# Performance work log

Hardware: AMD Instinct MI355X
Metric: run time of the kernel (lower is better)

Reference implementation:

```python
import jax, jax.numpy as jnp
import numpy as np

NUM_HEADS = 16
WINDOW = 512
EPS = 1e-5


def layer_norm(x, g, b):
    m = jnp.mean(x, axis=-1, keepdims=True)
    v = jnp.var(x, axis=-1, keepdims=True)
    return (x - m) * jax.lax.rsqrt(v + EPS) * g + b


def rope(x, pos):
    # x: [B,H,S,D], rotate-half RoPE with base 10000
    D = x.shape[-1]
    inv_freq = 1.0 / (10000.0 ** (jnp.arange(0, D, 2, dtype=jnp.float32) / D))
    ang = pos[:, None].astype(jnp.float32) * inv_freq  # [S, D/2]
    cos = jnp.concatenate([jnp.cos(ang), jnp.cos(ang)], axis=-1)
    sin = jnp.concatenate([jnp.sin(ang), jnp.sin(ang)], axis=-1)
    x1, x2 = jnp.split(x, 2, axis=-1)
    rot = jnp.concatenate([-x2, x1], axis=-1)
    return x * cos + rot * sin


def setup_inputs() -> dict:
    key = jax.random.key(0)
    ks = jax.random.split(key, 8)
    B, S, Dm = 2, 2048, 1024
    Dff = 4 * Dm
    sc = 0.02
    return {
        'hidden_states': jax.random.normal(ks[0], (B, S, Dm), jnp.float32),
        'ln1_g': jnp.ones((Dm,), jnp.float32),
        'ln1_b': jnp.zeros((Dm,), jnp.float32),
        'wq': jax.random.normal(ks[1], (Dm, Dm), jnp.float32) * sc,
        'bq': jnp.zeros((Dm,), jnp.float32),
        'wk': jax.random.normal(ks[2], (Dm, Dm), jnp.float32) * sc,
        'bk': jnp.zeros((Dm,), jnp.float32),
        'wv': jax.random.normal(ks[3], (Dm, Dm), jnp.float32) * sc,
        'bv': jnp.zeros((Dm,), jnp.float32),
        'wo': jax.random.normal(ks[4], (Dm, Dm), jnp.float32) * sc,
        'bo': jnp.zeros((Dm,), jnp.float32),
        'ln2_g': jnp.ones((Dm,), jnp.float32),
        'ln2_b': jnp.zeros((Dm,), jnp.float32),
        'w1': jax.random.normal(ks[5], (Dm, Dff), jnp.float32) * sc,
        'b1': jnp.zeros((Dff,), jnp.float32),
        'w2': jax.random.normal(ks[6], (Dff, Dm), jnp.float32) * sc,
        'b2': jnp.zeros((Dm,), jnp.float32),
        'global_token_indices': jax.random.randint(ks[7], (8,), 0, S, jnp.int32),
    }


def reference(hidden_states, ln1_g, ln1_b, wq, bq, wk, bk, wv, bv, wo, bo,
              ln2_g, ln2_b, w1, b1, w2, b2, global_token_indices):
    B, S, Dm = hidden_states.shape
    H = NUM_HEADS
    Dh = Dm // H

    # --- attention block ---
    x = layer_norm(hidden_states, ln1_g, ln1_b)
    heads = lambda t: t.reshape(B, S, H, Dh).transpose(0, 2, 1, 3)  # [B,H,S,Dh]
    q = heads(x @ wq + bq)
    k = heads(x @ wk + bk)
    v = heads(x @ wv + bv)

    pos = jnp.arange(S)
    q = rope(q, pos)
    k = rope(k, pos)

    scores = jnp.einsum('bhqd,bhkd->bhqk', q, k) / jnp.sqrt(jnp.float32(Dh))
    i = pos[:, None]
    j = pos[None, :]
    causal = j <= i
    band = causal & ((i - j) < WINDOW)
    is_global = jnp.zeros((S,), bool).at[global_token_indices].set(True)
    allowed = band | (causal & (is_global[None, :] | is_global[:, None]))
    scores = jnp.where(allowed[None, None], scores, jnp.float32(-1e9))
    attn = jax.nn.softmax(scores, axis=-1)
    ctx = jnp.einsum('bhqk,bhkd->bhqd', attn, v)
    ctx = ctx.transpose(0, 2, 1, 3).reshape(B, S, Dm)
    attn_out = ctx @ wo + bo
    h = hidden_states + attn_out

    # --- MLP block ---
    y = layer_norm(h, ln2_g, ln2_b)
    mlp = jax.nn.gelu(y @ w1 + b1, approximate=False) @ w2 + b2
    return h + mlp
```

## Files before the change

kernel.cpp:

```cpp
#include <hip/hip_runtime.h>

typedef unsigned short u16;
typedef __bf16 bf16x8 __attribute__((ext_vector_type(8)));
typedef short s16x8 __attribute__((ext_vector_type(8)));
typedef float f32x4 __attribute__((ext_vector_type(4)));

#define NB 2
#define SS 2048
#define DM 1024
#define NH 16
#define DH 64
#define DFF 4096

__device__ __forceinline__ u16 f2bf(float f) {
    unsigned u = __float_as_uint(f);
    u += 0x7fff + ((u >> 16) & 1);
    return (u16)(u >> 16);
}
__device__ __forceinline__ float bf2f(u16 h) {
    return __uint_as_float(((unsigned)h) << 16);
}
__device__ __forceinline__ void gld_lds16(const void* g, void* l) {
    __builtin_amdgcn_global_load_lds(
        (const __attribute__((address_space(1))) unsigned int*)(size_t)g,
        (__attribute__((address_space(3))) unsigned int*)(unsigned)(size_t)l,
        16, 0, 0);
}
__device__ __forceinline__ float gelu_f(float x) {
    return 0.5f * x * (1.f + erff(x * 0.70710678118654752f));
}

__global__ void wtrans_kernel(const float* __restrict__ w, u16* __restrict__ wt,
                              int K, int N) {
    __shared__ unsigned tl[64][65];
    int n0 = blockIdx.x * 64, k0 = blockIdx.y * 64, t = threadIdx.x;
    for (int it = 0; it < 16; ++it) {
        int e = it * 256 + t; int r = e >> 6, c = e & 63;
        tl[r][c] = f2bf(w[(size_t)(k0 + r) * N + n0 + c]);
    }
    __syncthreads();
    for (int it = 0; it < 16; ++it) {
        int e = it * 256 + t; int r = e >> 6, c = e & 63;
        wt[(size_t)(n0 + r) * K + k0 + c] = (u16)tl[c][r];
    }
}

__global__ void wtrans4_kernel(const float* __restrict__ a, const float* __restrict__ b,
                               const float* __restrict__ c, const float* __restrict__ d,
                               u16* __restrict__ oa, u16* __restrict__ ob,
                               u16* __restrict__ oc, u16* __restrict__ od) {
    __shared__ unsigned tl[64][65];
    const float* w; u16* wt;
    switch (blockIdx.z) {
        case 0: w = a; wt = oa; break;
        case 1: w = b; wt = ob; break;
        case 2: w = c; wt = oc; break;
        default: w = d; wt = od; break;
    }
    int n0 = blockIdx.x * 64, k0 = blockIdx.y * 64, t = threadIdx.x;
    for (int it = 0; it < 16; ++it) {
        int e = it * 256 + t; int r = e >> 6, cc = e & 63;
        tl[r][cc] = f2bf(w[(size_t)(k0 + r) * DM + n0 + cc]);
    }
    __syncthreads();
    for (int it = 0; it < 16; ++it) {
        int e = it * 256 + t; int r = e >> 6, cc = e & 63;
        wt[(size_t)(n0 + r) * DM + k0 + cc] = (u16)tl[cc][r];
    }
}

__global__ void build_aux(const int* __restrict__ gti, unsigned long long* __restrict__ kmask,
                          const float* __restrict__ bq, const float* __restrict__ bk,
                          const float* __restrict__ bv, float* __restrict__ bias3) {
    int t = threadIdx.x;
    if (t < 32) {
        unsigned long long m = 0ull;
        #pragma unroll
        for (int i = 0; i < 8; ++i) {
            int g = gti[i];
            if ((g >> 6) == t) m |= 1ull << (g & 63);
        }
        kmask[t] = m;
    }
    for (int i = t; i < 1024; i += 256) {
        bias3[i] = bq[i]; bias3[1024 + i] = bk[i]; bias3[2048 + i] = bv[i];
    }
}

template <bool INIT>
__global__ __launch_bounds__(256) void ln_kernel(const float* __restrict__ x,
                                                 const float* __restrict__ g,
                                                 const float* __restrict__ b,
                                                 u16* __restrict__ out,
                                                 const float* __restrict__ ib,
                                                 float* __restrict__ iout) {
    int row = blockIdx.x, t = threadIdx.x;
    const float4 v = ((const float4*)(x + (size_t)row * DM))[t];
    float s  = v.x + v.y + v.z + v.w;
    float sq = v.x * v.x + v.y * v.y + v.z * v.z + v.w * v.w;
    #pragma unroll
    for (int m = 1; m < 64; m <<= 1) { s += __shfl_xor(s, m); sq += __shfl_xor(sq, m); }
    __shared__ float ss[4], ssq[4];
    int wv = t >> 6, lane = t & 63;
    if (lane == 0) { ss[wv] = s; ssq[wv] = sq; }
    __syncthreads();
    s  = ss[0] + ss[1] + ss[2] + ss[3];
    sq = ssq[0] + ssq[1] + ssq[2] + ssq[3];
    float mean = s * (1.f / DM);
    float var  = sq * (1.f / DM) - mean * mean;
    float rs   = rsqrtf(var + 1e-5f);
    float4 gg = ((const float4*)g)[t];
    float4 bb = ((const float4*)b)[t];
    ushort4 o;
    o.x = f2bf((v.x - mean) * rs * gg.x + bb.x);
    o.y = f2bf((v.y - mean) * rs * gg.y + bb.y);
    o.z = f2bf((v.z - mean) * rs * gg.z + bb.z);
    o.w = f2bf((v.w - mean) * rs * gg.w + bb.w);
    ((ushort4*)(out + (size_t)row * DM))[t] = o;
    if (INIT) {
        float4 b2 = ((const float4*)ib)[t];
        float4 iv; iv.x = v.x + b2.x; iv.y = v.y + b2.y; iv.z = v.z + b2.z; iv.w = v.w + b2.w;
        ((float4*)(iout + (size_t)row * DM))[t] = iv;
    }
}

__global__ __launch_bounds__(256) void rope_kernel(const u16* __restrict__ qkv,
                                                   u16* __restrict__ qh,
                                                   u16* __restrict__ kh) {
    int idx = blockIdx.x * 256 + threadIdx.x;
    int d = idx & 31;
    int s = (idx >> 5) & (SS - 1);
    int h = (idx >> 16) & (NH - 1);
    int b = idx >> 20;
    size_t src = ((size_t)(b * SS + s)) * 3072 + h * DH + d;
    size_t dst = ((size_t)((b * NH + h) * SS + s)) * DH + d;
    float inv = powf(10000.f, -(float)d * (1.f / 32.f));
    float ang = (float)s * inv;
    float sn, cs;
    sincosf(ang, &sn, &cs);
    const float QSC = 0.125f;
    float x1 = bf2f(qkv[src]), x2 = bf2f(qkv[src + 32]);
    qh[dst]      = f2bf((x1 * cs - x2 * sn) * QSC);
    qh[dst + 32] = f2bf((x2 * cs + x1 * sn) * QSC);
    x1 = bf2f(qkv[src + 1024]); x2 = bf2f(qkv[src + 1024 + 32]);
    kh[dst]      = f2bf(x1 * cs - x2 * sn);
    kh[dst + 32] = f2bf(x2 * cs + x1 * sn);
}

__global__ __launch_bounds__(256) void vtrans_kernel(const u16* __restrict__ qkv,
                                                     u16* __restrict__ vt) {
    __shared__ unsigned tile[64][65];
    int st = blockIdx.x, bh = blockIdx.y;
    int b = bh >> 4, h = bh & 15, t = threadIdx.x;
    const u16* src = qkv + ((size_t)b * SS + st * 64) * 3072 + 2048 + h * DH;
    for (int it = 0; it < 16; ++it) {
        int e = it * 256 + t; int r = e >> 6, c = e & 63;
        tile[r][c] = src[(size_t)r * 3072 + c];
    }
    __syncthreads();
    u16* dst = vt + ((size_t)bh * DH) * SS + st * 64;
    for (int it = 0; it < 16; ++it) {
        int e = it * 256 + t; int d = e >> 6, s = e & 63;
        dst[(size_t)d * SS + s] = (u16)tile[s][d];
    }
}

__device__ __forceinline__ void xcd_remap(int& bn, int& bm, int& bz) {
    int s = blockIdx.x + gridDim.x * (blockIdx.y + gridDim.y * blockIdx.z);
    int q = gridDim.y >> 3;
    int xcd = s & 7, lin = s >> 3;
    bm = xcd * q + (lin % q);
    int rest = lin / q;
    bn = rest % gridDim.x;
    bz = rest / gridDim.x;
}

template <int MODE, int REMAP>
__global__ __launch_bounds__(256) void gemm_bt(const u16* __restrict__ A,
                                               const u16* __restrict__ Bt,
                                               const float* __restrict__ bias,
                                               const float* __restrict__ res,
                                               void* __restrict__ Cout,
                                               int M, int N, int K, int ldk) {
    int bnb = blockIdx.x, bmb = blockIdx.y, bzb = blockIdx.z;
    if (REMAP) xcd_remap(bnb, bmb, bzb);
    const int bm = bmb * 128, bn = bnb * 128;
    const int koff = bzb * K;
    const int t = threadIdx.x, wv = t >> 6, lane = t & 63;
    const int lr = lane & 15, lq = lane >> 4;
    const int wm = (wv >> 1) * 64, wn = (wv & 1) * 64;
    __shared__ __align__(16) u16 As[2][128 * 64];
    __shared__ __align__(16) u16 Bs[2][128 * 64];
    f32x4 acc[4][4] = {};

    auto stage = [&](int kb, int buf) {
        #pragma unroll
        for (int p = 0; p < 4; ++p) {
            int c = p * 256 + t;
            int r = c >> 3;
            int gc = ((c & 7) ^ (r & 7)) * 8;
            gld_lds16(A + (size_t)(bm + r) * ldk + kb + gc,
                      As[buf] + (size_t)(p * 256 + wv * 64) * 8);
            gld_lds16(Bt + (size_t)(bn + r) * ldk + kb + gc,
                      Bs[buf] + (size_t)(p * 256 + wv * 64) * 8);
        }
    };

    stage(koff, 0);
    int pb = 0;
    for (int k0 = 0; k0 < K; k0 += 64) {
        __syncthreads();
        if (k0 + 64 < K) stage(koff + k0 + 64, pb ^ 1);
        const u16* Ac = As[pb];
        const u16* Bc = Bs[pb];
        #pragma unroll
        for (int ks = 0; ks < 2; ++ks) {
            bf16x8 af[4], bfr[4];
            #pragma unroll
            for (int mi = 0; mi < 4; ++mi) {
                int row = wm + mi * 16 + lr;
                af[mi] = *(const bf16x8*)&Ac[row * 64 + (((ks * 4 + lq) ^ (row & 7)) * 8)];
            }
            #pragma unroll
            for (int ni = 0; ni < 4; ++ni) {
                int row = wn + ni * 16 + lr;
                bfr[ni] = *(const bf16x8*)&Bc[row * 64 + (((ks * 4 + lq) ^ (row & 7)) * 8)];
            }
            #pragma unroll
            for (int mi = 0; mi < 4; ++mi)
                #pragma unroll
                for (int ni = 0; ni < 4; ++ni)
                    acc[mi][ni] = __builtin_amdgcn_mfma_f32_16x16x32_bf16(af[mi], bfr[ni], acc[mi][ni], 0, 0, 0);
        }
        pb ^= 1;
    }
    #pragma unroll
    for (int mi = 0; mi < 4; ++mi) {
        int row0 = bm + wm + mi * 16 + lq * 4;
        #pragma unroll
        for (int ni = 0; ni < 4; ++ni) {
            int col = bn + wn + ni * 16 + lr;
            float bv = (MODE == 3) ? 0.f : bias[col];
            #pragma unroll
            for (int r = 0; r < 4; ++r) {
                float v = acc[mi][ni][r] + bv;
                size_t off = (size_t)(row0 + r) * N + col;
                if (MODE == 1) v += res[off];
                if (MODE == 2) v = gelu_f(v);
                if (MODE == 0 || MODE == 2) ((u16*)Cout)[off] = f2bf(v);
                else if (MODE == 1)         ((float*)Cout)[off] = v;
                else                        atomicAdd((float*)Cout + off, v);
            }
        }
    }
}

template <int MODE, int REMAP>
__global__ __launch_bounds__(512, 2) void gemm256(const u16* __restrict__ A,
                                                  const u16* __restrict__ Bt,
                                                  const float* __restrict__ bias,
                                                  void* __restrict__ Cout,
                                                  int M, int N, int K, int ldk) {
    int bnb = blockIdx.x, bmb = blockIdx.y, bzb = blockIdx.z;
    if (REMAP) xcd_remap(bnb, bmb, bzb);
    const int bm = bmb * 256, bn = bnb * 256;
    const int t = threadIdx.x, wv = t >> 6, lane = t & 63;
    const int lr = lane & 15, lq = lane >> 4;
    const int wm = (wv >> 2) * 128, wn = (wv & 3) * 64;
    const int awb = (wv >> 2) * 64;
    const int bwb = (wv & 3) * 32;
    __shared__ __align__(16) u16 As[2 * 2 * 128 * 64];
    __shared__ __align__(16) u16 Bs[2 * 2 * 128 * 64];
    f32x4 acc[8][4] = {};
    bf16x8 aA[4][2], bA[2][2], bB[2][2];

    const int aix0 = (awb + lr) * 64 + ((lq ^ (lr & 7)) * 8);
    const int aix1 = aix0 ^ 32;
    const int bix0 = (bwb + lr) * 64 + ((lq ^ (lr & 7)) * 8);
    const int bix1 = bix0 ^ 32;

    const u16 *pAsrc[2][2], *pBsrc[2][2];
    #pragma unroll
    for (int g = 0; g < 2; ++g)
        #pragma unroll
        for (int p = 0; p < 2; ++p) {
            int c = p * 512 + t;
            int glr = c >> 3, sl = c & 7;
            int sc = (sl ^ (glr & 7)) * 8;
            int grA = (glr & 63) + g * 64 + ((glr >> 6) << 7);
            int grB = (glr & 31) + g * 32 + ((glr >> 5) << 6);
            pAsrc[g][p] = A  + (size_t)(bm + grA) * ldk + sc;
            pBsrc[g][p] = Bt + (size_t)(bn + grB) * ldk + sc;
        }
    auto stA = [&](int g, int db, int ku) {
        #pragma unroll
        for (int p = 0; p < 2; ++p)
            gld_lds16(pAsrc[g][p] + ku, As + (size_t)(db * 2 + g) * 8192
                                           + (size_t)(p * 512 + wv * 64) * 8);
    };
    auto stB = [&](int g, int db, int ku) {
        #pragma unroll
        for (int p = 0; p < 2; ++p)
            gld_lds16(pBsrc[g][p] + ku, Bs + (size_t)(db * 2 + g) * 8192
                                           + (size_t)(p * 512 + wv * 64) * 8);
    };
    auto mmac = [&](int qm, int qn, bf16x8 (&bb)[2][2]) {
        __builtin_amdgcn_s_setprio(1);
        #pragma unroll
        for (int mi2 = 0; mi2 < 4; ++mi2)
            #pragma unroll
            for (int ni2 = 0; ni2 < 2; ++ni2)
                #pragma unroll
                for (int ks = 0; ks < 2; ++ks)
                    acc[qm * 4 + mi2][qn * 2 + ni2] =
                        __builtin_amdgcn_mfma_f32_16x16x32_bf16(
                            aA[mi2][ks], bb[ni2][ks], acc[qm * 4 + mi2][qn * 2 + ni2], 0, 0, 0);
        __builtin_amdgcn_s_setprio(0);
    };
    #define BAR       __builtin_amdgcn_s_barrier()
    #define VMW(n)    asm volatile("s_waitcnt vmcnt(" #n ")" ::: "memory")
    #define LOADA(DB, G) do {                                                  \
        constexpr int O_ = ((DB) * 2 + (G)) * 8192;                            \
        aA[0][0] = *(const bf16x8*)&As[aix0 + O_];                             \
        aA[0][1] = *(const bf16x8*)&As[aix1 + O_];                             \
        aA[1][0] = *(const bf16x8*)&As[aix0 + O_ + 1024];                      \
        aA[1][1] = *(const bf16x8*)&As[aix1 + O_ + 1024];                      \
        aA[2][0] = *(const bf16x8*)&As[aix0 + O_ + 2048];                      \
        aA[2][1] = *(const bf16x8*)&As[aix1 + O_ + 2048];                      \
        aA[3][0] = *(const bf16x8*)&As[aix0 + O_ + 3072];                      \
        aA[3][1] = *(const bf16x8*)&As[aix1 + O_ + 3072];                      \
    } while (0)
    #define LOADB(DB, G, DST) do {                                             \
        constexpr int O_ = ((DB) * 2 + (G)) * 8192;                            \
        DST[0][0] = *(const bf16x8*)&Bs[bix0 + O_];                            \
        DST[0][1] = *(const bf16x8*)&Bs[bix1 + O_];                            \
        DST[1][0] = *(const bf16x8*)&Bs[bix0 + O_ + 1024];                     \
        DST[1][1] = *(const bf16x8*)&Bs[bix1 + O_ + 1024];                     \
    } while (0)
    #define G256_TILE(DB, KT) do {                                             \
        const int ku1 = ((KT) + 1) << 6, ku2 = ((KT) + 2) << 6;                \
        LOADA(DB, 0); LOADB(DB, 0, bA);               \
        stA(1, (DB) ^ 1, ku1);                                                 \
        BAR;                                                                   \
        mmac(0, 0, bA);                                                        \
        VMW(6); BAR;                                                           \
        LOADB(DB, 1, bB);                             \
        stB(1, (DB) ^ 1, ku1);                                                 \
        BAR;                                                                   \
        mmac(0, 1, bB);                                                        \
        BAR;                                                                   \
        LOADA(DB, 1);                                 \
        stA(0, DB, ku2);                                                       \
        BAR;                                                                   \
        mmac(1, 1, bB);                                                        \
        BAR;                                                                   \
        stB(0, DB, ku2);                              \
        BAR;                                                                   \
        mmac(1, 0, bA);                                                        \
        VMW(8); BAR;                                                           \
    } while (0)

    const int NT = K >> 6;
    stA(0, 0, 0); stB(0, 0, 0); stA(1, 0, 0); stB(1, 0, 0);
    stA(0, 1, 64); stB(0, 1, 64);
    VMW(8);
    BAR;

    for (int kt = 0; kt + 4 <= NT; kt += 2) {
        G256_TILE(0, kt);
        G256_TILE(1, kt + 1);
    }
    {
        const int ku1 = (NT - 1) << 6;
        LOADA(0, 0); LOADB(0, 0, bA);
        stA(1, 1, ku1);
        BAR;
        mmac(0, 0, bA);
        VMW(6);
        BAR;
        LOADB(0, 1, bB);
        stB(1, 1, ku1);
        BAR;
        mmac(0, 1, bB);
        BAR;
        LOADA(0, 1);
        BAR;
        mmac(1, 1, bB);
        BAR;
        mmac(1, 0, bA);
        VMW(4);
        BAR;
    }
    {
        LOADA(1, 0); LOADB(1, 0, bA);
        BAR;
        mmac(0, 0, bA);
        VMW(0);
        BAR;
        LOADB(1, 1, bB);
        BAR;
        mmac(0, 1, bB);
        BAR;
        LOADA(1, 1);
        BAR;
        mmac(1, 1, bB);
        mmac(1, 0, bA);
    }
    #undef G256_TILE
    #undef LOADA
    #undef LOADB
    #undef BAR
    #undef VMW

    #pragma unroll
    for (int mi = 0; mi < 8; ++mi) {
        int row0 = bm + wm + mi * 16 + lq * 4;
        #pragma unroll
        for (int ni = 0; ni < 4; ++ni) {
            int col = bn + wn + ni * 16 + lr;
            float bv = bias[col];
            #pragma unroll
            for (int r = 0; r < 4; ++r) {
                float v = acc[mi][ni][r] + bv;
                size_t off = (size_t)(row0 + r) * N + col;
                if (MODE == 2) v = gelu_f(v);
                ((u16*)Cout)[off] = f2bf(v);
            }
        }
    }
}

__global__ __launch_bounds__(256) void attn_kernel(const u16* __restrict__ qh,
                                                   const u16* __restrict__ kh,
                                                   const u16* __restrict__ vt,
                                                   const unsigned long long* __restrict__ kmask,
                                                   u16* __restrict__ ctx) {
    const int qt = blockIdx.x, bh = blockIdx.y;
    const int b = bh >> 4, h = bh & 15;
    const int t = threadIdx.x, wv = t >> 6, lane = t & 63;
    const int lr = lane & 15, lq = lane >> 4;
    const int q0 = qt * 64;

    __shared__ __align__(16) u16 Qs[64 * 64];
    __shared__ __align__(16) u16 Ks[2][64 * 64];
    __shared__ __align__(16) u16 Vs[2][64 * 64];
    __shared__ __align__(16) u16 Ps[64 * 64];

    const u16* qbase = qh + ((size_t)bh * SS) * DH;
    const u16* kbase = kh + ((size_t)bh * SS) * DH;
    const u16* vbase = vt + ((size_t)bh * DH) * SS;

    #pragma unroll
    for (int p = 0; p < 2; ++p) {
        int c = p * 256 + t; int r = c >> 3, sl = c & 7;
        gld_lds16(qbase + (size_t)(q0 + r) * DH + ((sl ^ (r & 7)) * 8),
                  Qs + (size_t)(p * 256 + wv * 64) * 8);
    }

    float sum_part[4] = {0.f, 0.f, 0.f, 0.f};
    f32x4 acc_o[4] = {};

    const int lim = qt - 8;
    int cur = 0;
    while (cur < lim && kmask[cur] == 0ull) ++cur;
    {
        int k0 = cur * 64;
        #pragma unroll
        for (int p = 0; p < 2; ++p) {
            int c = p * 256 + t; int r = c >> 3; int gc = ((c & 7) ^ (r & 7)) * 8;
            gld_lds16(kbase + (size_t)(k0 + r) * DH + gc, Ks[0] + (size_t)(p * 256 + wv * 64) * 8);
            gld_lds16(vbase + (size_t)r * SS + k0 + gc,  Vs[0] + (size_t)(p * 256 + wv * 64) * 8);
        }
    }
    __syncthreads();
    bf16x8 qf[2];
    {
        const int arow = wv * 16 + lr;
        qf[0] = *(const bf16x8*)&Qs[arow * 64 + (((0 * 4 + lq) ^ (arow & 7)) * 8)];
        qf[1] = *(const bf16x8*)&Qs[arow * 64 + (((1 * 4 + lq) ^ (arow & 7)) * 8)];
    }
    int pb = 0;
    while (cur >= 0) {
        int nxt = cur + 1;
        while (nxt < lim && kmask[nxt] == 0ull) ++nxt;
        if (nxt > qt) nxt = -1;
        __syncthreads();
        if (nxt >= 0) {
            int k0n = nxt * 64;
            #pragma unroll
            for (int p = 0; p < 2; ++p) {
                int c = p * 256 + t; int r = c >> 3; int gc = ((c & 7) ^ (r & 7)) * 8;
                gld_lds16(kbase + (size_t)(k0n + r) * DH + gc, Ks[pb ^ 1] + (size_t)(p * 256 + wv * 64) * 8);
                gld_lds16(vbase + (size_t)r * SS + k0n + gc,  Vs[pb ^ 1] + (size_t)(p * 256 + wv * 64) * 8);
            }
        }
        const u16* Kt = Ks[pb];
        const u16* Vt = Vs[pb];
        const int k0 = cur * 64;

        f32x4 s_acc[4] = {};
        __builtin_amdgcn_s_setprio(1);
        #pragma unroll
        for (int ks = 0; ks < 2; ++ks) {
            #pragma unroll
            for (int ni = 0; ni < 4; ++ni) {
                const int brow = ni * 16 + lr;
                bf16x8 bfr = *(const bf16x8*)&Kt[brow * 64 + (((ks * 4 + lq) ^ (brow & 7)) * 8)];
                s_acc[ni] = __builtin_amdgcn_mfma_f32_16x16x32_bf16(qf[ks], bfr, s_acc[ni], 0, 0, 0);
            }
        }
        __builtin_amdgcn_s_setprio(0);
        float sv[4][4];
        if (cur >= qt - 7 && cur != qt) {
            #pragma unroll
            for (int ni = 0; ni < 4; ++ni)
                #pragma unroll
                for (int r = 0; r < 4; ++r) sv[ni][r] = __expf(s_acc[ni][r]);
        } else if (cur == qt) {
            #pragma unroll
            for (int ni = 0; ni < 4; ++ni) {
                int j = ni * 16 + lr;
                #pragma unroll
                for (int r = 0; r < 4; ++r) {
                    int i = wv * 16 + lq * 4 + r;
                    float p = __expf(s_acc[ni][r]);
                    sv[ni][r] = (j <= i) ? p : 0.f;
                }
            }
        } else {
            unsigned long long cm = kmask[cur];
            #pragma unroll
            for (int ni = 0; ni < 4; ++ni) {
                int j = k0 + ni * 16 + lr;
                bool gj = (cm >> (ni * 16 + lr)) & 1ull;
                #pragma unroll
                for (int r = 0; r < 4; ++r) {
                    int i = q0 + wv * 16 + lq * 4 + r;
                    bool ok = ((i - j) < 512) | gj;
                    float p = __expf(s_acc[ni][r]);
                    sv[ni][r] = ok ? p : 0.f;
                }
            }
        }
        #pragma unroll
        for (int ni = 0; ni < 4; ++ni) {
            int col = ni * 16 + lr;
            #pragma unroll
            for (int r = 0; r < 4; ++r) {
                int row = wv * 16 + lq * 4 + r;
                sum_part[r] += sv[ni][r];
                Ps[row * 64 + (((col >> 3) ^ (row & 7)) * 8) + (col & 7)] = f2bf(sv[ni][r]);
            }
        }
        __builtin_amdgcn_s_setprio(1);
        #pragma unroll
        for (int ks = 0; ks < 2; ++ks) {
            const int arow = wv * 16 + lr;
            bf16x8 af = *(const bf16x8*)&Ps[arow * 64 + (((ks * 4 + lq) ^ (arow & 7)) * 8)];
            #pragma unroll
            for (int ni = 0; ni < 4; ++ni) {
                const int brow = ni * 16 + lr;
                bf16x8 bfr = *(const bf16x8*)&Vt[brow * 64 + (((ks * 4 + lq) ^ (brow & 7)) * 8)];
                acc_o[ni] = __builtin_amdgcn_mfma_f32_16x16x32_bf16(af, bfr, acc_o[ni], 0, 0, 0);
            }
        }
        __builtin_amdgcn_s_setprio(0);
        cur = nxt; pb ^= 1;
    }
    float inv_l[4];
    #pragma unroll
    for (int r = 0; r < 4; ++r) {
        float ls = sum_part[r];
        #pragma unroll
        for (int m = 1; m < 16; m <<= 1) ls += __shfl_xor(ls, m, 16);
        inv_l[r] = 1.f / ls;
    }
    u16* obase = ctx + ((size_t)b * SS) * DM + h * DH;
    #pragma unroll
    for (int ni = 0; ni < 4; ++ni)
        #pragma unroll
        for (int r = 0; r < 4; ++r) {
            int i = q0 + wv * 16 + lq * 4 + r;
            obase[(size_t)i * DM + ni * 16 + lr] = f2bf(acc_o[ni][r] * inv_l[r]);
        }
}

__global__ __launch_bounds__(256) void attn_fix_kernel(const u16* __restrict__ qh,
                                                       const u16* __restrict__ kh,
                                                       const u16* __restrict__ qkv,
                                                       const int* __restrict__ gti,
                                                       u16* __restrict__ ctx) {
    const int gidx = blockIdx.x, bh = blockIdx.y;
    const int b = bh >> 4, h = bh & 15;
    const int t = threadIdx.x, wv = t >> 6, lane = t & 63;
    const int i = gti[gidx];

    __shared__ float qsh[64];
    if (t < 64) qsh[t] = bf2f(qh[((size_t)bh * SS + i) * DH + t]);
    __syncthreads();
    float qreg[64];
    #pragma unroll
    for (int c = 0; c < 16; ++c) {
        float4 qv = ((const float4*)qsh)[c];
        qreg[c * 4 + 0] = qv.x; qreg[c * 4 + 1] = qv.y;
        qreg[c * 4 + 2] = qv.z; qreg[c * 4 + 3] = qv.w;
    }

    const u16* kb = kh + (size_t)bh * SS * DH;
    const u16* vb = qkv + (size_t)b * SS * 3072 + 2048 + h * DH;

    float Oacc[64];
    #pragma unroll
    for (int d = 0; d < 64; ++d) Oacc[d] = 0.f;
    float lacc = 0.f;

    for (int j0 = wv * 64; j0 <= i; j0 += 256) {
        const int j = j0 + lane;
        const bool valid = (j <= i);
        const int jc = valid ? j : i;
        const s16x8* krow = (const s16x8*)(kb + (size_t)jc * DH);
        float part[8];
        #pragma unroll
        for (int c = 0; c < 8; ++c) {
            s16x8 kv = krow[c];
            float p0 = 0.f;
            #pragma unroll
            for (int e = 0; e < 8; ++e) p0 += qreg[c * 8 + e] * bf2f((u16)kv[e]);
            part[c] = p0;
        }
        float s = ((part[0] + part[1]) + (part[2] + part[3])) +
                  ((part[4] + part[5]) + (part[6] + part[7]));
        const float p = valid ? __expf(s) : 0.f;
        lacc += p;
        const s16x8* vrow = (const s16x8*)(vb + (size_t)jc * 3072);
        #pragma unroll
        for (int c = 0; c < 8; ++c) {
            s16x8 vv = vrow[c];
            #pragma unroll
            for (int e = 0; e < 8; ++e) Oacc[c * 8 + e] += p * bf2f((u16)vv[e]);
        }
    }
    #pragma unroll
    for (int m = 1; m < 64; m <<= 1) {
        lacc += __shfl_xor(lacc, m);
        #pragma unroll
        for (int d = 0; d < 64; ++d) Oacc[d] += __shfl_xor(Oacc[d], m);
    }
    float out = 0.f;
    #pragma unroll
    for (int d = 0; d < 64; ++d) out = (lane == d) ? Oacc[d] : out;
    __shared__ float osum[4][64];
    __shared__ float lsum[4];
    osum[wv][lane] = out;
    if (lane == 0) lsum[wv] = lacc;
    __syncthreads();
    if (wv == 0) {
        float ot = osum[0][lane] + osum[1][lane] + osum[2][lane] + osum[3][lane];
        float lt = lsum[0] + lsum[1] + lsum[2] + lsum[3];
        ctx[((size_t)b * SS + i) * DM + h * DH + lane] = f2bf(ot / lt);
    }
}

extern "C" void kernel_launch(void* const* d_in, const int* in_sizes, int n_in,
                              void* d_out, int out_size, void* d_ws, size_t ws_size,
                              hipStream_t stream) {
    (void)in_sizes; (void)n_in; (void)out_size; (void)ws_size;
    const float* hidden = (const float*)d_in[0];
    const float* ln1_g  = (const float*)d_in[1];
    const float* ln1_b  = (const float*)d_in[2];
    const float* wq = (const float*)d_in[3];  const float* bq = (const float*)d_in[4];
    const float* wk = (const float*)d_in[5];  const float* bk = (const float*)d_in[6];
    const float* wv = (const float*)d_in[7];  const float* bv = (const float*)d_in[8];
    const float* wo = (const float*)d_in[9];  const float* bo = (const float*)d_in[10];
    const float* ln2_g = (const float*)d_in[11];
    const float* ln2_b = (const float*)d_in[12];
    const float* w1 = (const float*)d_in[13]; const float* b1 = (const float*)d_in[14];
    const float* w2 = (const float*)d_in[15]; const float* b2 = (const float*)d_in[16];
    const int*  gti = (const int*)d_in[17];

    char* ws = (char*)d_ws;
    const size_t MB = 1u << 20;
    u16* wqt  = (u16*)(ws + 0 * MB);
    u16* wkt  = (u16*)(ws + 2 * MB);
    u16* wvt  = (u16*)(ws + 4 * MB);
    u16* wot  = (u16*)(ws + 6 * MB);
    u16* w1t  = (u16*)(ws + 8 * MB);
    u16* w2t  = (u16*)(ws + 16 * MB);
    u16* xb   = (u16*)(ws + 24 * MB);
    u16* ctx  = xb;
    u16* qkv  = (u16*)(ws + 32 * MB);
    u16* qhb  = (u16*)(ws + 56 * MB);
    u16* khb  = (u16*)(ws + 64 * MB);
    u16* vtb  = (u16*)(ws + 72 * MB);
    float* hb = (float*)(ws + 80 * MB);
    u16* act  = (u16*)(ws + 32 * MB);
    u16* yb   = (u16*)(ws + 64 * MB);
    unsigned long long* kmask = (unsigned long long*)(ws + 96 * MB);
    float* bias3 = (float*)(ws + 96 * MB + 8192);

    wtrans4_kernel<<<dim3(16, 16, 4), 256, 0, stream>>>(wq, wk, wv, wo, wqt, wkt, wvt, wot);
    wtrans_kernel<<<dim3(64, 16), 256, 0, stream>>>(w1, w1t, DM, DFF);
    wtrans_kernel<<<dim3(16, 64), 256, 0, stream>>>(w2, w2t, DFF, DM);
    build_aux<<<1, 256, 0, stream>>>(gti, kmask, bq, bk, bv, bias3);

    ln_kernel<false><<<NB * SS, 256, 0, stream>>>(hidden, ln1_g, ln1_b, xb, nullptr, nullptr);

    gemm256<0, 1><<<dim3(3072 / 256, (NB * SS) / 256), 512, 0, stream>>>(
        xb, wqt, bias3, qkv, NB * SS, 3072, DM, DM);

    rope_kernel<<<(NB * NH * SS * 32) / 256, 256, 0, stream>>>(qkv, qhb, khb);
    vtrans_kernel<<<dim3(SS / 64, NB * NH), 256, 0, stream>>>(qkv, vtb);

    attn_kernel<<<dim3(SS / 64, NB * NH), 256, 0, stream>>>(qhb, khb, vtb, kmask, ctx);
    attn_fix_kernel<<<dim3(8, NB * NH), 256, 0, stream>>>(qhb, khb, qkv, gti, ctx);

    gemm_bt<1, 1><<<dim3(8, 32), 256, 0, stream>>>(ctx, wot, bo, hidden, hb, NB * SS, DM, DM, DM);
    ln_kernel<true><<<NB * SS, 256, 0, stream>>>(hb, ln2_g, ln2_b, yb, b2, (float*)d_out);
    gemm256<2, 1><<<dim3(DFF / 256, (NB * SS) / 256), 512, 0, stream>>>(
        yb, w1t, b1, act, NB * SS, DFF, DM, DM);
    gemm_bt<3, 1><<<dim3(8, 32, 2), 256, 0, stream>>>(act, w2t, nullptr, nullptr, d_out, NB * SS, DM, DFF / 2, DFF);
}
```

Baseline: 384.5 us.

## Enlarge attention query tile to 128 rows per block for K/V reuse

The attention kernel now handles 128 query rows per block, with each wave computing two 16-row fragments. Every K/V tile loaded into LDS is therefore reused for twice as many queries, which halves the global K/V traffic and the loop overhead per query. The masking conditions are rewritten for the larger tile: the last two key tiles get the causal mask and the band tiles are adjusted. In exchange the grid has half as many blocks (512), register and LDS use go up, and more wasted work is done on partially masked tiles, which may hurt occupancy and load balance.

```diff
diff --git a/kernel.cpp b/kernel.cpp
--- a/kernel.cpp
+++ b/kernel.cpp
@@ -439,28 +439,29 @@
     const int b = bh >> 4, h = bh & 15;
     const int t = threadIdx.x, wv = t >> 6, lane = t & 63;
     const int lr = lane & 15, lq = lane >> 4;
-    const int q0 = qt * 64;
-
-    __shared__ __align__(16) u16 Qs[64 * 64];
+    const int q0 = qt * 128;
+
+    __shared__ __align__(16) u16 Qs[128 * 64];
     __shared__ __align__(16) u16 Ks[2][64 * 64];
     __shared__ __align__(16) u16 Vs[2][64 * 64];
-    __shared__ __align__(16) u16 Ps[64 * 64];
+    __shared__ __align__(16) u16 Ps[128 * 64];
 
     const u16* qbase = qh + ((size_t)bh * SS) * DH;
     const u16* kbase = kh + ((size_t)bh * SS) * DH;
     const u16* vbase = vt + ((size_t)bh * DH) * SS;
 
     #pragma unroll
-    for (int p = 0; p < 2; ++p) {
+    for (int p = 0; p < 4; ++p) {
         int c = p * 256 + t; int r = c >> 3, sl = c & 7;
         gld_lds16(qbase + (size_t)(q0 + r) * DH + ((sl ^ (r & 7)) * 8),
                   Qs + (size_t)(p * 256 + wv * 64) * 8);
     }
 
-    float sum_part[4] = {0.f, 0.f, 0.f, 0.f};
-    f32x4 acc_o[4] = {};
-
-    const int lim = qt - 8;
+    float sum_part[2][4] = {};
+    f32x4 acc_o[2][4] = {};
+
+    const int kend = 2 * qt + 1;
+    const int lim = (2 * qt - 8 > 0) ? (2 * qt - 8) : 0;
     int cur = 0;
     while (cur < lim && kmask[cur] == 0ull) ++cur;
     {
@@ -473,17 +474,18 @@
         }
     }
     __syncthreads();
-    bf16x8 qf[2];
-    {
-        const int arow = wv * 16 + lr;
-        qf[0] = *(const bf16x8*)&Qs[arow * 64 + (((0 * 4 + lq) ^ (arow & 7)) * 8)];
-        qf[1] = *(const bf16x8*)&Qs[arow * 64 + (((1 * 4 + lq) ^ (arow & 7)) * 8)];
+    bf16x8 qf[2][2];
+    #pragma unroll
+    for (int f = 0; f < 2; ++f) {
+        const int arow = wv * 32 + f * 16 + lr;
+        qf[f][0] = *(const bf16x8*)&Qs[arow * 64 + (((0 * 4 + lq) ^ (arow & 7)) * 8)];
+        qf[f][1] = *(const bf16x8*)&Qs[arow * 64 + (((1 * 4 + lq) ^ (arow & 7)) * 8)];
     }
     int pb = 0;
     while (cur >= 0) {
         int nxt = cur + 1;
         while (nxt < lim && kmask[nxt] == 0ull) ++nxt;
-        if (nxt > qt) nxt = -1;
+        if (nxt > kend) nxt = -1;
         __syncthreads();
         if (nxt >= 0) {
             int k0n = nxt * 64;
@@ -498,7 +500,7 @@
         const u16* Vt = Vs[pb];
         const int k0 = cur * 64;
 
-        f32x4 s_acc[4] = {};
+        f32x4 s_acc[2][4] = {};
         __builtin_amdgcn_s_setprio(1);
         #pragma unroll
         for (int ks = 0; ks < 2; ++ks) {
@@ -506,83 +508,100 @@
             for (int ni = 0; ni < 4; ++ni) {
                 const int brow = ni * 16 + lr;
                 bf16x8 bfr = *(const bf16x8*)&Kt[brow * 64 + (((ks * 4 + lq) ^ (brow & 7)) * 8)];
-                s_acc[ni] = __builtin_amdgcn_mfma_f32_16x16x32_bf16(qf[ks], bfr, s_acc[ni], 0, 0, 0);
+                #pragma unroll
+                for (int f = 0; f < 2; ++f)
+                    s_acc[f][ni] = __builtin_amdgcn_mfma_f32_16x16x32_bf16(qf[f][ks], bfr, s_acc[f][ni], 0, 0, 0);
             }
         }
         __builtin_amdgcn_s_setprio(0);
-        float sv[4][4];
-        if (cur >= qt - 7 && cur != qt) {
-            #pragma unroll
-            for (int ni = 0; ni < 4; ++ni)
+        float sv[2][4][4];
+        if (cur >= 2 * qt) {
+            #pragma unroll
+            for (int f = 0; f < 2; ++f)
                 #pragma unroll
-                for (int r = 0; r < 4; ++r) sv[ni][r] = __expf(s_acc[ni][r]);
-        } else if (cur == qt) {
+                for (int ni = 0; ni < 4; ++ni) {
+                    int j = k0 + ni * 16 + lr;
+                    #pragma unroll
+                    for (int r = 0; r < 4; ++r) {
+                        int i = q0 + wv * 32 + f * 16 + lq * 4 + r;
+                        float p = __expf(s_acc[f][ni][r]);
+                        sv[f][ni][r] = (j <= i) ? p : 0.f;
+                    }
+                }
+        } else if (cur >= 2 * qt - 6) {
+            #pragma unroll
+            for (int f = 0; f < 2; ++f)
+                #pragma unroll
+                for (int ni = 0; ni < 4; ++ni)
+                    #pragma unroll
+                    for (int r = 0; r < 4; ++r) sv[f][ni][r] = __expf(s_acc[f][ni][r]);
+        } else {
+            unsigned long long cm = kmask[cur];
+            #pragma unroll
+            for (int f = 0; f < 2; ++f)
+                #pragma unroll
+                for (int ni = 0; ni < 4; ++ni) {
+                    int j = k0 + ni * 16 + lr;
+                    bool gj = (cm >> (ni * 16 + lr)) & 1ull;
+                    #pragma unroll
+                    for (int r = 0; r < 4; ++r) {
+                        int i = q0 + wv * 32 + f * 16 + lq * 4 + r;
+                        bool ok = ((i - j) < 512) | gj;
+                        float p = __expf(s_acc[f][ni][r]);
+                        sv[f][ni][r] = ok ? p : 0.f;
+                    }
+                }
+        }
+        #pragma unroll
+        for (int f = 0; f < 2; ++f)
             #pragma unroll
             for (int ni = 0; ni < 4; ++ni) {
-                int j = ni * 16 + lr;
+                int col = ni * 16 + lr;
                 #pragma unroll
                 for (int r = 0; r < 4; ++r) {
-                    int i = wv * 16 + lq * 4 + r;
-                    float p = __expf(s_acc[ni][r]);
-                    sv[ni][r] = (j <= i) ? p : 0.f;
+                    int row = wv * 32 + f * 16 + lq * 4 + r;
+                    sum_part[f][r] += sv[f][ni][r];
+                    Ps[row * 64 + (((col >> 3) ^ (row & 7)) * 8) + (col & 7)] = f2bf(sv[f][ni][r]);
                 }
             }
-        } else {
-            unsigned long long cm = kmask[cur];
-            #pragma unroll
-            for (int ni = 0; ni < 4; ++ni) {
-                int j = k0 + ni * 16 + lr;
-                bool gj = (cm >> (ni * 16 + lr)) & 1ull;
+        __builtin_amdgcn_s_setprio(1);
+        #pragma unroll
+        for (int ks = 0; ks < 2; ++ks) {
+            #pragma unroll
+            for (int f = 0; f < 2; ++f) {
+                const int arow = wv * 32 + f * 16 + lr;
+                bf16x8 af = *(const bf16x8*)&Ps[arow * 64 + (((ks * 4 + lq) ^ (arow & 7)) * 8)];
                 #pragma unroll
-                for (int r = 0; r < 4; ++r) {
-                    int i = q0 + wv * 16 + lq * 4 + r;
-                    bool ok = ((i - j) < 512) | gj;
-                    float p = __expf(s_acc[ni][r]);
-                    sv[ni][r] = ok ? p : 0.f;
+                for (int ni = 0; ni < 4; ++ni) {
+                    const int brow = ni * 16 + lr;
+                    bf16x8 bfr = *(const bf16x8*)&Vt[brow * 64 + (((ks * 4 + lq) ^ (brow & 7)) * 8)];
+                    acc_o[f][ni] = __builtin_amdgcn_mfma_f32_16x16x32_bf16(af, bfr, acc_o[f][ni], 0, 0, 0);
                 }
-            }
-        }
-        #pragma unroll
-        for (int ni = 0; ni < 4; ++ni) {
-            int col = ni * 16 + lr;
-            #pragma unroll
-            for (int r = 0; r < 4; ++r) {
-                int row = wv * 16 + lq * 4 + r;
-                sum_part[r] += sv[ni][r];
-                Ps[row * 64 + (((col >> 3) ^ (row & 7)) * 8) + (col & 7)] = f2bf(sv[ni][r]);
-            }
-        }
-        __builtin_amdgcn_s_setprio(1);
-        #pragma unroll
-        for (int ks = 0; ks < 2; ++ks) {
-            const int arow = wv * 16 + lr;
-            bf16x8 af = *(const bf16x8*)&Ps[arow * 64 + (((ks * 4 + lq) ^ (arow & 7)) * 8)];
-            #pragma unroll
-            for (int ni = 0; ni < 4; ++ni) {
-                const int brow = ni * 16 + lr;
-                bf16x8 bfr = *(const bf16x8*)&Vt[brow * 64 + (((ks * 4 + lq) ^ (brow & 7)) * 8)];
-                acc_o[ni] = __builtin_amdgcn_mfma_f32_16x16x32_bf16(af, bfr, acc_o[ni], 0, 0, 0);
             }
         }
         __builtin_amdgcn_s_setprio(0);
         cur = nxt; pb ^= 1;
     }
-    float inv_l[4];
-    #pragma unroll
-    for (int r = 0; r < 4; ++r) {
-        float ls = sum_part[r];
-        #pragma unroll
-        for (int m = 1; m < 16; m <<= 1) ls += __shfl_xor(ls, m, 16);
-        inv_l[r] = 1.f / ls;
-    }
+    float inv_l[2][4];
+    #pragma unroll
+    for (int f = 0; f < 2; ++f)
+        #pragma unroll
+        for (int r = 0; r < 4; ++r) {
+            float ls = sum_part[f][r];
+            #pragma unroll
+            for (int m = 1; m < 16; m <<= 1) ls += __shfl_xor(ls, m, 16);
+            inv_l[f][r] = 1.f / ls;
+        }
     u16* obase = ctx + ((size_t)b * SS) * DM + h * DH;
     #pragma unroll
-    for (int ni = 0; ni < 4; ++ni)
-        #pragma unroll
-        for (int r = 0; r < 4; ++r) {
-            int i = q0 + wv * 16 + lq * 4 + r;
-            obase[(size_t)i * DM + ni * 16 + lr] = f2bf(acc_o[ni][r] * inv_l[r]);
-        }
+    for (int f = 0; f < 2; ++f)
+        #pragma unroll
+        for (int ni = 0; ni < 4; ++ni)
+            #pragma unroll
+            for (int r = 0; r < 4; ++r) {
+                int i = q0 + wv * 32 + f * 16 + lq * 4 + r;
+                obase[(size_t)i * DM + ni * 16 + lr] = f2bf(acc_o[f][ni][r] * inv_l[f][r]);
+            }
 }
 
 __global__ __launch_bounds__(256) void attn_fix_kernel(const u16* __restrict__ qh,
@@ -711,7 +730,7 @@
     rope_kernel<<<(NB * NH * SS * 32) / 256, 256, 0, stream>>>(qkv, qhb, khb);
     vtrans_kernel<<<dim3(SS / 64, NB * NH), 256, 0, stream>>>(qkv, vtb);
 
-    attn_kernel<<<dim3(SS / 64, NB * NH), 256, 0, stream>>>(qhb, khb, vtb, kmask, ctx);
+    attn_kernel<<<dim3(SS / 128, NB * NH), 256, 0, stream>>>(qhb, khb, vtb, kmask, ctx);
     attn_fix_kernel<<<dim3(8, NB * NH), 256, 0, stream>>>(qhb, khb, qkv, gti, ctx);
 
     gemm_bt<1, 1><<<dim3(8, 32), 256, 0, stream>>>(ctx, wot, bo, hidden, hb, NB * SS, DM, DM, DM);
```

After: 380.3 us. Within noise of the previous version (-1.1%).
